# Kernel optimization log

Hardware: AMD Instinct MI355X
Metric: run time of the kernel (lower is better)

The kernel has to match this reference:

```python
import jax, jax.numpy as jnp
import numpy as np

FLOOR = 1e-06
B, T, C = 64, 4096, 80


def _ema(x, w):
    """EMA a_t = w*x_t + (1-w)*a_{t-1}, a_{-1} = x[:,0], via parallel associative scan.
    x: [B,T,C], w: [C] (clipped to [0,1]). Returns [B,T,C].
    Note: with init = x[:,0], the first output is exactly x[:,0].
    """
    A = jnp.broadcast_to(1.0 - w, x.shape)          # decay per step
    b = w * x                                        # input injection per step
    # Fold the initial state into step 0: a_0 = w*x_0 + (1-w)*x_0 = x_0
    A = A.at[:, 0, :].set(0.0)
    b = b.at[:, 0, :].set(x[:, 0, :])

    def combine(c1, c2):
        A1, b1 = c1
        A2, b2 = c2
        return A1 * A2, A2 * b1 + b2

    _, ema = jax.lax.associative_scan(combine, (A, b), axis=1)
    return ema


def setup_inputs() -> dict:
    key = jax.random.key(0)
    k_in, = jax.random.split(key, 1)
    inputs = jax.random.uniform(k_in, (B, T, C), dtype=jnp.float32)  # non-negative energies
    alpha = jnp.full((C,), 0.96, dtype=jnp.float32)
    delta = jnp.full((C,), 2.0, dtype=jnp.float32)
    root = jnp.full((C,), 2.0, dtype=jnp.float32)
    smooth = jnp.full((C,), 0.04, dtype=jnp.float32)
    return {"inputs": inputs, "alpha": alpha, "delta": delta, "root": root, "smooth": smooth}


def reference(inputs, alpha, delta, root, smooth):
    w = jnp.clip(smooth, 0.0, 1.0)
    a = jnp.minimum(alpha, 1.0)
    r = jnp.maximum(root, 1.0)
    ema_smoother = _ema(inputs, w)                       # [B,T,C]
    one_over_root = 1.0 / r                              # [C]
    out = (inputs / (FLOOR + ema_smoother) ** a + delta) ** one_over_root - delta ** one_over_root
    return out
```

## Files before the change

### kernel.cpp

```cpp
#include <hip/hip_runtime.h>

#define FLOOR_EPS 1e-6f

typedef float f32x4 __attribute__((ext_vector_type(4)));

constexpr int Bn   = 64;
constexpr int Tn   = 4096;
constexpr int Cn   = 80;
constexpr int G    = Cn / 4;
constexpr int P    = 16;
constexpr int SLAB = Tn / P;
constexpr int KC   = 16;
constexpr int CH   = SLAB / KC;
constexpr int NT   = KC * G;
constexpr int SC2  = 2 * KC;

__device__ __forceinline__ void nt_store4(float4* p, float a, float b,
                                          float c, float d) {
    f32x4 v = {a, b, c, d};
    __builtin_nontemporal_store(v, (f32x4*)p);
}

__global__ __launch_bounds__(NT, 5)
void pcen_fused(const float* __restrict__ x,
                const float* __restrict__ alpha,
                const float* __restrict__ delta,
                const float* __restrict__ root,
                const float* __restrict__ smooth,
                float* __restrict__ out)
{
    __shared__ float4 sc[2][SC2][G];

    const int p  = blockIdx.x % P;
    const int b  = blockIdx.x / P;
    const int t  = threadIdx.x;
    const int g  = t % G;
    const int kc = t / G;

    const float4 smv = ((const float4*)smooth)[g];
    float w0 = fminf(fmaxf(smv.x, 0.f), 1.f), w1 = fminf(fmaxf(smv.y, 0.f), 1.f);
    float w2 = fminf(fmaxf(smv.z, 0.f), 1.f), w3 = fminf(fmaxf(smv.w, 0.f), 1.f);
    float d0 = 1.f - w0, d1 = 1.f - w1, d2 = 1.f - w2, d3 = 1.f - w3;

    float q0 = d0 * d0, q1 = d1 * d1, q2 = d2 * d2, q3 = d3 * d3;
    q0 *= q0; q1 *= q1; q2 *= q2; q3 *= q3;
    q0 *= q0; q1 *= q1; q2 *= q2; q3 *= q3;
    q0 *= q0; q1 *= q1; q2 *= q2; q3 *= q3;

    const size_t rowbase = ((size_t)b * Tn + (size_t)p * SLAB + (size_t)kc * CH) * G + g;
    const float4* px = (const float4*)x + rowbase;

    const bool fc = (p == 0) && (kc == 0);
    float eP0 = 0.f, eP1 = 0.f, eP2 = 0.f, eP3 = 0.f;
    float eO0, eO1, eO2, eO3;
    if (fc) { float4 v = px[0]; eO0 = v.x; eO1 = v.y; eO2 = v.z; eO3 = v.w; }
    else    { eO0 = 0.f; eO1 = 0.f; eO2 = 0.f; eO3 = 0.f; }

    if (p > 0) {
        const float4* pw = px - (size_t)SLAB * G;
        #pragma unroll
        for (int u = 0; u < CH; ++u) {
            float4 a = pw[(size_t)u * G];
            float4 v = px[(size_t)u * G];
            eP0 = fmaf(d0, eP0, w0 * a.x);
            eP1 = fmaf(d1, eP1, w1 * a.y);
            eP2 = fmaf(d2, eP2, w2 * a.z);
            eP3 = fmaf(d3, eP3, w3 * a.w);
            eO0 = fmaf(d0, eO0, w0 * v.x);
            eO1 = fmaf(d1, eO1, w1 * v.y);
            eO2 = fmaf(d2, eO2, w2 * v.z);
            eO3 = fmaf(d3, eO3, w3 * v.w);
        }
    } else {
        #pragma unroll
        for (int u = 0; u < CH; ++u) {
            float4 v = px[(size_t)u * G];
            eO0 = fmaf(d0, eO0, w0 * v.x);
            eO1 = fmaf(d1, eO1, w1 * v.y);
            eO2 = fmaf(d2, eO2, w2 * v.z);
            eO3 = fmaf(d3, eO3, w3 * v.w);
        }
    }
    sc[0][kc][g]      = make_float4(eP0, eP1, eP2, eP3);
    sc[0][KC + kc][g] = make_float4(eO0, eO1, eO2, eO3);
    __syncthreads();

    float W0 = q0, W1 = q1, W2 = q2, W3 = q3;
    int src = 0;
    #pragma unroll
    for (int off = 1; off < SC2; off <<= 1) {
        float4 v1 = sc[src][kc][g];
        float4 v2 = sc[src][KC + kc][g];
        if (kc >= off) {
            float4 u4 = sc[src][kc - off][g];
            v1.x = fmaf(W0, u4.x, v1.x);
            v1.y = fmaf(W1, u4.y, v1.y);
            v1.z = fmaf(W2, u4.z, v1.z);
            v1.w = fmaf(W3, u4.w, v1.w);
        }
        {
            float4 u4 = sc[src][KC + kc - off][g];
            v2.x = fmaf(W0, u4.x, v2.x);
            v2.y = fmaf(W1, u4.y, v2.y);
            v2.z = fmaf(W2, u4.z, v2.z);
            v2.w = fmaf(W3, u4.w, v2.w);
        }
        sc[src ^ 1][kc][g]      = v1;
        sc[src ^ 1][KC + kc][g] = v2;
        __syncthreads();
        src ^= 1;
        W0 *= W0; W1 *= W1; W2 *= W2; W3 *= W3;
    }

    float4 ex = sc[src][KC - 1 + kc][g];
    float m0 = ex.x, m1 = ex.y, m2 = ex.z, m3 = ex.w;
    if (fc) { float4 v = px[0]; m0 = v.x; m1 = v.y; m2 = v.z; m3 = v.w; }

    const float4 alv = ((const float4*)alpha)[g];
    const float4 dlv = ((const float4*)delta)[g];
    const float4 rov = ((const float4*)root)[g];
    float nega[4], invr[4], dl[4], sub[4];
    {
        float as[4] = {alv.x, alv.y, alv.z, alv.w};
        float rs[4] = {rov.x, rov.y, rov.z, rov.w};
        dl[0] = dlv.x; dl[1] = dlv.y; dl[2] = dlv.z; dl[3] = dlv.w;
        #pragma unroll
        for (int j = 0; j < 4; ++j) {
            nega[j] = -fminf(as[j], 1.f);
            invr[j] = 1.f / fmaxf(rs[j], 1.f);
            sub[j]  = __expf(invr[j] * __logf(dl[j]));
        }
    }
    const bool all_sqrt = (invr[0] == 0.5f) & (invr[1] == 0.5f) &
                          (invr[2] == 0.5f) & (invr[3] == 0.5f);

    asm volatile("" ::: "memory");

    float4* po = (float4*)out + rowbase;

    if (all_sqrt) {
        #pragma unroll
        for (int u = 0; u < CH; ++u) {
            float4 xv = px[(size_t)u * G];
            m0 = fmaf(d0, m0, w0 * xv.x);
            m1 = fmaf(d1, m1, w1 * xv.y);
            m2 = fmaf(d2, m2, w2 * xv.z);
            m3 = fmaf(d3, m3, w3 * xv.w);
            nt_store4(&po[(size_t)u * G],
                sqrtf(fmaf(xv.x, __expf(nega[0] * __logf(FLOOR_EPS + m0)), dl[0])) - sub[0],
                sqrtf(fmaf(xv.y, __expf(nega[1] * __logf(FLOOR_EPS + m1)), dl[1])) - sub[1],
                sqrtf(fmaf(xv.z, __expf(nega[2] * __logf(FLOOR_EPS + m2)), dl[2])) - sub[2],
                sqrtf(fmaf(xv.w, __expf(nega[3] * __logf(FLOOR_EPS + m3)), dl[3])) - sub[3]);
        }
    } else {
        float w[4] = {w0, w1, w2, w3}, dc[4] = {d0, d1, d2, d3};
        float mm[4] = {m0, m1, m2, m3};
        #pragma unroll
        for (int u = 0; u < CH; ++u) {
            float4 xv = px[(size_t)u * G];
            float xv4[4] = {xv.x, xv.y, xv.z, xv.w};
            float os[4];
            #pragma unroll
            for (int j = 0; j < 4; ++j) {
                mm[j]   = fmaf(dc[j], mm[j], w[j] * xv4[j]);
                float pw = __expf(nega[j] * __logf(FLOOR_EPS + mm[j]));
                float v  = fmaf(xv4[j], pw, dl[j]);
                os[j]    = __expf(invr[j] * __logf(v)) - sub[j];
            }
            nt_store4(&po[(size_t)u * G], os[0], os[1], os[2], os[3]);
        }
    }
}

extern "C" void kernel_launch(void* const* d_in, const int* in_sizes, int n_in,
                              void* d_out, int out_size, void* d_ws, size_t ws_size,
                              hipStream_t stream) {
    const float* x      = (const float*)d_in[0];
    const float* alpha  = (const float*)d_in[1];
    const float* delta  = (const float*)d_in[2];
    const float* root   = (const float*)d_in[3];
    const float* smooth = (const float*)d_in[4];
    float* out = (float*)d_out;

    pcen_fused<<<Bn * P, NT, 0, stream>>>(x, alpha, delta, root, smooth, out);
}
```

Baseline: 176.2 us.

## Double time slabs per batch, extend warmup to two prior slabs, remap blocks across XCDs

```diff
diff --git a/kernel.cpp b/kernel.cpp
--- a/kernel.cpp
+++ b/kernel.cpp
@@ -8,12 +8,14 @@
 constexpr int Tn   = 4096;
 constexpr int Cn   = 80;
 constexpr int G    = Cn / 4;
-constexpr int P    = 16;
+constexpr int P    = 32;
 constexpr int SLAB = Tn / P;
 constexpr int KC   = 16;
 constexpr int CH   = SLAB / KC;
 constexpr int NT   = KC * G;
-constexpr int SC2  = 2 * KC;
+constexpr int SCN  = 3 * KC;
+constexpr int NWG  = Bn * P;
+constexpr int NXCD = 8;
 
 __device__ __forceinline__ void nt_store4(float4* p, float a, float b,
                                           float c, float d) {
@@ -29,10 +31,11 @@
                 const float* __restrict__ smooth,
                 float* __restrict__ out)
 {
-    __shared__ float4 sc[2][SC2][G];
-
-    const int p  = blockIdx.x % P;
-    const int b  = blockIdx.x / P;
+    __shared__ float4 sc[2][SCN][G];
+
+    const int lin = ((int)blockIdx.x % NXCD) * (NWG / NXCD) + (int)blockIdx.x / NXCD;
+    const int p  = lin % P;
+    const int b  = lin / P;
     const int t  = threadIdx.x;
     const int g  = t % G;
     const int kc = t / G;
@@ -45,52 +48,79 @@
     float q0 = d0 * d0, q1 = d1 * d1, q2 = d2 * d2, q3 = d3 * d3;
     q0 *= q0; q1 *= q1; q2 *= q2; q3 *= q3;
     q0 *= q0; q1 *= q1; q2 *= q2; q3 *= q3;
-    q0 *= q0; q1 *= q1; q2 *= q2; q3 *= q3;
 
     const size_t rowbase = ((size_t)b * Tn + (size_t)p * SLAB + (size_t)kc * CH) * G + g;
-    const float4* px = (const float4*)x + rowbase;
+    const float4* px  = (const float4*)x + rowbase;
+    const float4* pw1 = px - (size_t)SLAB * G;
+    const float4* pw2 = px - (size_t)2 * SLAB * G;
 
     const bool fc = (p == 0) && (kc == 0);
-    float eP0 = 0.f, eP1 = 0.f, eP2 = 0.f, eP3 = 0.f;
-    float eO0, eO1, eO2, eO3;
-    if (fc) { float4 v = px[0]; eO0 = v.x; eO1 = v.y; eO2 = v.z; eO3 = v.w; }
-    else    { eO0 = 0.f; eO1 = 0.f; eO2 = 0.f; eO3 = 0.f; }
-
-    if (p > 0) {
-        const float4* pw = px - (size_t)SLAB * G;
-        #pragma unroll
-        for (int u = 0; u < CH; ++u) {
-            float4 a = pw[(size_t)u * G];
+    float eA0 = 0.f, eA1 = 0.f, eA2 = 0.f, eA3 = 0.f;
+    float eB0 = 0.f, eB1 = 0.f, eB2 = 0.f, eB3 = 0.f;
+    float eC0 = 0.f, eC1 = 0.f, eC2 = 0.f, eC3 = 0.f;
+    if (fc) { float4 v = px[0]; eC0 = v.x; eC1 = v.y; eC2 = v.z; eC3 = v.w; }
+
+    if (p >= 2) {
+        if (p == 2 && kc == 0) {
+            float4 v = pw2[0]; eA0 = v.x; eA1 = v.y; eA2 = v.z; eA3 = v.w;
+        }
+        #pragma unroll
+        for (int u = 0; u < CH; ++u) {
+            float4 a = pw2[(size_t)u * G];
+            float4 c = pw1[(size_t)u * G];
             float4 v = px[(size_t)u * G];
-            eP0 = fmaf(d0, eP0, w0 * a.x);
-            eP1 = fmaf(d1, eP1, w1 * a.y);
-            eP2 = fmaf(d2, eP2, w2 * a.z);
-            eP3 = fmaf(d3, eP3, w3 * a.w);
-            eO0 = fmaf(d0, eO0, w0 * v.x);
-            eO1 = fmaf(d1, eO1, w1 * v.y);
-            eO2 = fmaf(d2, eO2, w2 * v.z);
-            eO3 = fmaf(d3, eO3, w3 * v.w);
+            eA0 = fmaf(d0, eA0, w0 * a.x);
+            eA1 = fmaf(d1, eA1, w1 * a.y);
+            eA2 = fmaf(d2, eA2, w2 * a.z);
+            eA3 = fmaf(d3, eA3, w3 * a.w);
+            eB0 = fmaf(d0, eB0, w0 * c.x);
+            eB1 = fmaf(d1, eB1, w1 * c.y);
+            eB2 = fmaf(d2, eB2, w2 * c.z);
+            eB3 = fmaf(d3, eB3, w3 * c.w);
+            eC0 = fmaf(d0, eC0, w0 * v.x);
+            eC1 = fmaf(d1, eC1, w1 * v.y);
+            eC2 = fmaf(d2, eC2, w2 * v.z);
+            eC3 = fmaf(d3, eC3, w3 * v.w);
+        }
+    } else if (p == 1) {
+        if (kc == 0) {
+            float4 v = pw1[0]; eB0 = v.x; eB1 = v.y; eB2 = v.z; eB3 = v.w;
+        }
+        #pragma unroll
+        for (int u = 0; u < CH; ++u) {
+            float4 c = pw1[(size_t)u * G];
+            float4 v = px[(size_t)u * G];
+            eB0 = fmaf(d0, eB0, w0 * c.x);
+            eB1 = fmaf(d1, eB1, w1 * c.y);
+            eB2 = fmaf(d2, eB2, w2 * c.z);
+            eB3 = fmaf(d3, eB3, w3 * c.w);
+            eC0 = fmaf(d0, eC0, w0 * v.x);
+            eC1 = fmaf(d1, eC1, w1 * v.y);
+            eC2 = fmaf(d2, eC2, w2 * v.z);
+            eC3 = fmaf(d3, eC3, w3 * v.w);
         }
     } else {
         #pragma unroll
         for (int u = 0; u < CH; ++u) {
             float4 v = px[(size_t)u * G];
-            eO0 = fmaf(d0, eO0, w0 * v.x);
-            eO1 = fmaf(d1, eO1, w1 * v.y);
-            eO2 = fmaf(d2, eO2, w2 * v.z);
-            eO3 = fmaf(d3, eO3, w3 * v.w);
-        }
-    }
-    sc[0][kc][g]      = make_float4(eP0, eP1, eP2, eP3);
-    sc[0][KC + kc][g] = make_float4(eO0, eO1, eO2, eO3);
+            eC0 = fmaf(d0, eC0, w0 * v.x);
+            eC1 = fmaf(d1, eC1, w1 * v.y);
+            eC2 = fmaf(d2, eC2, w2 * v.z);
+            eC3 = fmaf(d3, eC3, w3 * v.w);
+        }
+    }
+    sc[0][kc][g]          = make_float4(eA0, eA1, eA2, eA3);
+    sc[0][KC + kc][g]     = make_float4(eB0, eB1, eB2, eB3);
+    sc[0][2 * KC + kc][g] = make_float4(eC0, eC1, eC2, eC3);
     __syncthreads();
 
     float W0 = q0, W1 = q1, W2 = q2, W3 = q3;
     int src = 0;
     #pragma unroll
-    for (int off = 1; off < SC2; off <<= 1) {
+    for (int off = 1; off < SCN; off <<= 1) {
         float4 v1 = sc[src][kc][g];
         float4 v2 = sc[src][KC + kc][g];
+        float4 v3 = sc[src][2 * KC + kc][g];
         if (kc >= off) {
             float4 u4 = sc[src][kc - off][g];
             v1.x = fmaf(W0, u4.x, v1.x);
@@ -98,21 +128,29 @@
             v1.z = fmaf(W2, u4.z, v1.z);
             v1.w = fmaf(W3, u4.w, v1.w);
         }
-        {
+        if (off <= KC) {
             float4 u4 = sc[src][KC + kc - off][g];
             v2.x = fmaf(W0, u4.x, v2.x);
             v2.y = fmaf(W1, u4.y, v2.y);
             v2.z = fmaf(W2, u4.z, v2.z);
             v2.w = fmaf(W3, u4.w, v2.w);
         }
-        sc[src ^ 1][kc][g]      = v1;
-        sc[src ^ 1][KC + kc][g] = v2;
+        {
+            float4 u4 = sc[src][2 * KC + kc - off][g];
+            v3.x = fmaf(W0, u4.x, v3.x);
+            v3.y = fmaf(W1, u4.y, v3.y);
+            v3.z = fmaf(W2, u4.z, v3.z);
+            v3.w = fmaf(W3, u4.w, v3.w);
+        }
+        sc[src ^ 1][kc][g]          = v1;
+        sc[src ^ 1][KC + kc][g]     = v2;
+        sc[src ^ 1][2 * KC + kc][g] = v3;
         __syncthreads();
         src ^= 1;
         W0 *= W0; W1 *= W1; W2 *= W2; W3 *= W3;
     }
 
-    float4 ex = sc[src][KC - 1 + kc][g];
+    float4 ex = sc[src][2 * KC - 1 + kc][g];
     float m0 = ex.x, m1 = ex.y, m2 = ex.z, m3 = ex.w;
     if (fc) { float4 v = px[0]; m0 = v.x; m1 = v.y; m2 = v.z; m3 = v.w; }
 
@@ -182,5 +220,5 @@
     const float* smooth = (const float*)d_in[4];
     float* out = (float*)d_out;
 
-    pcen_fused<<<Bn * P, NT, 0, stream>>>(x, alpha, delta, root, smooth, out);
+    pcen_fused<<<NWG, NT, 0, stream>>>(x, alpha, delta, root, smooth, out);
 }
```

New measurement: 182.1 us. 3.3% more time.
